# Optimization experiments

Hardware: AMD Instinct MI355X
Metric: run time of the kernel (lower is better)

## Reference

```python
import jax, jax.numpy as jnp
import numpy as np
import math

N_NODES = 50000
N_EDGES = 800000
HIDDEN = 128
NUM_GAUSS = 50
NUM_FILTERS = 128
CUTOFF = 10.0
SHIFT = math.log(2.0)


def setup_inputs() -> dict:
    key = jax.random.key(0)
    ks = jax.random.split(key, 12)
    x = jax.random.normal(ks[0], (N_NODES, HIDDEN), dtype=jnp.float32)
    edge_index = jax.random.randint(ks[1], (2, N_EDGES), 0, N_NODES, dtype=jnp.int64)
    edge_weight = jax.random.uniform(ks[2], (N_EDGES,), dtype=jnp.float32)
    edge_attr = jax.random.normal(ks[3], (N_EDGES, NUM_GAUSS), dtype=jnp.float32)
    # learned parameters (xavier-ish scale)
    def xavier(k, shape):
        fan_in, fan_out = shape[1], shape[0]
        bound = math.sqrt(6.0 / (fan_in + fan_out))
        return jax.random.uniform(k, shape, dtype=jnp.float32, minval=-bound, maxval=bound)
    mlp_w1 = xavier(ks[4], (NUM_FILTERS, NUM_GAUSS))
    mlp_b1 = jnp.zeros((NUM_FILTERS,), jnp.float32)
    mlp_w2 = xavier(ks[5], (NUM_FILTERS, NUM_FILTERS))
    mlp_b2 = jnp.zeros((NUM_FILTERS,), jnp.float32)
    lin1_w = xavier(ks[6], (NUM_FILTERS, HIDDEN))   # no bias
    lin2_w = xavier(ks[7], (HIDDEN, NUM_FILTERS))
    lin2_b = jnp.zeros((HIDDEN,), jnp.float32)
    lin_w = xavier(ks[8], (HIDDEN, HIDDEN))
    lin_b = jnp.zeros((HIDDEN,), jnp.float32)
    return {"x": x, "edge_index": edge_index, "edge_weight": edge_weight,
            "edge_attr": edge_attr, "mlp_w1": mlp_w1, "mlp_b1": mlp_b1,
            "mlp_w2": mlp_w2, "mlp_b2": mlp_b2, "lin1_w": lin1_w,
            "lin2_w": lin2_w, "lin2_b": lin2_b, "lin_w": lin_w, "lin_b": lin_b}


def shifted_softplus(v):
    return jax.nn.softplus(v) - SHIFT


def reference(x, edge_index, edge_weight, edge_attr, mlp_w1, mlp_b1,
              mlp_w2, mlp_b2, lin1_w, lin2_w, lin2_b, lin_w, lin_b):
    src, dst = edge_index[0], edge_index[1]
    # cosine cutoff per edge: [E]
    C = 0.5 * (jnp.cos(edge_weight * (jnp.pi / CUTOFF)) + 1.0)
    # edge filter MLP: [E, num_filters]
    h_e = shifted_softplus(edge_attr @ mlp_w1.T + mlp_b1)
    W = (h_e @ mlp_w2.T + mlp_b2) * C[:, None]
    # node projection, gather-multiply-scatter aggregation
    h = x @ lin1_w.T                       # [N, num_filters]
    msg = h[src] * W                       # [E, num_filters]
    agg = jax.ops.segment_sum(msg, dst, num_segments=N_NODES)  # [N, num_filters]
    h = agg @ lin2_w.T + lin2_b            # [N, hidden]
    h = shifted_softplus(h)
    out = h @ lin_w.T + lin_b              # [N, hidden]
    return out
```

## Files before the change

kernel.cpp:

```cpp
#include <hip/hip_runtime.h>
#include <hip/hip_bf16.h>
#include <math.h>

#define E_NUM 800000
#define NN 50000
#define NG 50
#define NTW (E_NUM / 16)
#define EDGE_BLOCKS 768

typedef __bf16 bf16x8 __attribute__((ext_vector_type(8)));
typedef float f32x4 __attribute__((ext_vector_type(4)));
typedef unsigned short ushortx8 __attribute__((ext_vector_type(8)));

__device__ __forceinline__ unsigned short f2b(float f) {
  union { __bf16 h; unsigned short u; } v; v.h = (__bf16)f; return v.u;
}
__device__ __forceinline__ float b2f(unsigned short u) {
  union { unsigned u; float f; } v; v.u = ((unsigned)u) << 16; return v.f;
}
__device__ __forceinline__ float sspf(float v) {
  float e = __builtin_amdgcn_exp2f(-1.4426950408889634f * fabsf(v));
  return fmaxf(v, 0.f) + 0.6931471805599453f * __builtin_amdgcn_logf(fmaf(0.5f, e, 0.5f));
}

__global__ __launch_bounds__(256) void k_hist(const int* __restrict__ ei, int* __restrict__ counts) {
  int e = blockIdx.x * 256 + threadIdx.x;
  if (e < E_NUM) atomicAdd(&counts[ei[E_NUM + e]], 1);
}

__global__ __launch_bounds__(1024) void k_scan(const int* __restrict__ counts,
                                               int* __restrict__ cursor, int* __restrict__ off) {
  __shared__ int tot[1024];
  const int t = threadIdx.x;
  const int C = (NN + 1023) >> 10;
  int lo = t * C, hi = lo + C; if (hi > NN) hi = NN; if (lo > NN) lo = NN;
  int s = 0;
  for (int i = lo; i < hi; ++i) s += counts[i];
  tot[t] = s;
  __syncthreads();
  int mine = s;
  for (int o = 1; o < 1024; o <<= 1) {
    int v = (t >= o) ? tot[t - o] : 0;
    __syncthreads();
    tot[t] += v;
    __syncthreads();
  }
  int run = tot[t] - mine;
  for (int i = lo; i < hi; ++i) { int c = counts[i]; cursor[i] = run; off[i] = run; run += c; }
  if (t == 1023) off[NN] = E_NUM;
}

__global__ __launch_bounds__(256) void k_scatter2(const int* __restrict__ ei,
                                                  int* __restrict__ cursor,
                                                  int* __restrict__ srcS, int* __restrict__ dstS,
                                                  int* __restrict__ eS) {
  int e = blockIdx.x * 256 + threadIdx.x;
  if (e < E_NUM) {
    int d = ei[E_NUM + e];
    int pos = atomicAdd(&cursor[d], 1);
    srcS[pos] = ei[e];
    dstS[pos] = d;
    eS[pos] = e;
  }
}

__global__ __launch_bounds__(256) void k_mfma_gemm(
    const float* __restrict__ X, const float* __restrict__ Wm,
    const float* __restrict__ bias, float* __restrict__ out, int act, int nrows)
{
  __shared__ __attribute__((aligned(16))) unsigned short s_x[128 * 128];
  __shared__ __attribute__((aligned(16))) unsigned short s_w[128 * 128];
  const int tid = threadIdx.x;
  const int w = tid >> 6, lane = tid & 63, q = lane >> 4, n16 = lane & 15;
  const int base = blockIdx.x * 128;

  for (int c = tid; c < 128 * 16; c += 256) {
    int f = c >> 4, ch = c & 15;
    const float4* wp = (const float4*)(Wm + f * 128 + ch * 8);
    float4 v0 = wp[0], v1 = wp[1];
    ushortx8 v = { f2b(v0.x), f2b(v0.y), f2b(v0.z), f2b(v0.w),
                   f2b(v1.x), f2b(v1.y), f2b(v1.z), f2b(v1.w) };
    *(ushortx8*)&s_w[(f << 7) + ((ch ^ (f & 15)) << 3)] = v;
  }
  for (int c = tid; c < 128 * 16; c += 256) {
    int r = c >> 4, ch = c & 15;
    int n = base + r;
    float4 v0 = {0.f, 0.f, 0.f, 0.f}, v1 = v0;
    if (n < nrows) {
      const float4* xp = (const float4*)(X + (long)n * 128 + ch * 8);
      v0 = xp[0]; v1 = xp[1];
    }
    ushortx8 v = { f2b(v0.x), f2b(v0.y), f2b(v0.z), f2b(v0.w),
                   f2b(v1.x), f2b(v1.y), f2b(v1.z), f2b(v1.w) };
    *(ushortx8*)&s_x[(r << 7) + ((ch ^ (r & 15)) << 3)] = v;
  }
  __syncthreads();

  float bv[8];
#pragma unroll
  for (int t = 0; t < 8; ++t) bv[t] = bias ? bias[t * 16 + n16] : 0.f;

  bf16x8 a[2][4];
#pragma unroll
  for (int g = 0; g < 2; ++g) {
    int r = w * 32 + g * 16 + n16;
#pragma unroll
    for (int ks = 0; ks < 4; ++ks)
      a[g][ks] = *(const bf16x8*)&s_x[(r << 7) + (((ks * 4 + q) ^ (r & 15)) << 3)];
  }
#pragma unroll
  for (int t = 0; t < 8; ++t) {
    int f = t * 16 + n16;
    bf16x8 b[4];
#pragma unroll
    for (int ks = 0; ks < 4; ++ks)
      b[ks] = *(const bf16x8*)&s_w[(f << 7) + (((ks * 4 + q) ^ (f & 15)) << 3)];
#pragma unroll
    for (int g = 0; g < 2; ++g) {
      f32x4 acc = {0.f, 0.f, 0.f, 0.f};
#pragma unroll
      for (int ks = 0; ks < 4; ++ks)
        acc = __builtin_amdgcn_mfma_f32_16x16x32_bf16(a[g][ks], b[ks], acc, 0, 0, 0);
#pragma unroll
      for (int r = 0; r < 4; ++r) {
        int n = base + w * 32 + g * 16 + q * 4 + r;
        if (n < nrows) {
          float v = acc[r] + bv[t];
          if (act) v = sspf(v);
          out[(long)n * 128 + f] = v;
        }
      }
    }
  }
}

__global__ __launch_bounds__(256, 2) void k_gemm23(
    const float* __restrict__ A, const float* __restrict__ W2,
    const float* __restrict__ B2, const float* __restrict__ W3,
    const float* __restrict__ B3, float* __restrict__ out, int nrows)
{
  __shared__ __attribute__((aligned(16))) unsigned short s_x[128 * 128];
  __shared__ __attribute__((aligned(16))) unsigned short s_w[128 * 128];
  const int tid = threadIdx.x;
  const int w = tid >> 6, lane = tid & 63, q = lane >> 4, n16 = lane & 15;
  const int base = blockIdx.x * 128;

  for (int c = tid; c < 128 * 16; c += 256) {
    int f = c >> 4, ch = c & 15;
    const float4* wp = (const float4*)(W2 + f * 128 + ch * 8);
    float4 v0 = wp[0], v1 = wp[1];
    ushortx8 v = { f2b(v0.x), f2b(v0.y), f2b(v0.z), f2b(v0.w),
                   f2b(v1.x), f2b(v1.y), f2b(v1.z), f2b(v1.w) };
    *(ushortx8*)&s_w[(f << 7) + ((ch ^ (f & 15)) << 3)] = v;
  }
  for (int c = tid; c < 128 * 16; c += 256) {
    int r = c >> 4, ch = c & 15;
    int n = base + r;
    float4 v0 = {0.f, 0.f, 0.f, 0.f}, v1 = v0;
    if (n < nrows) {
      const float4* xp = (const float4*)(A + (long)n * 128 + ch * 8);
      v0 = xp[0]; v1 = xp[1];
    }
    ushortx8 v = { f2b(v0.x), f2b(v0.y), f2b(v0.z), f2b(v0.w),
                   f2b(v1.x), f2b(v1.y), f2b(v1.z), f2b(v1.w) };
    *(ushortx8*)&s_x[(r << 7) + ((ch ^ (r & 15)) << 3)] = v;
  }
  __syncthreads();

  float b2v[8], b3v[8];
#pragma unroll
  for (int t = 0; t < 8; ++t) { b2v[t] = B2[t * 16 + n16]; b3v[t] = B3[t * 16 + n16]; }

  bf16x8 a[2][4];
#pragma unroll
  for (int g = 0; g < 2; ++g) {
    int r = w * 32 + g * 16 + n16;
#pragma unroll
    for (int ks = 0; ks < 4; ++ks)
      a[g][ks] = *(const bf16x8*)&s_x[(r << 7) + (((ks * 4 + q) ^ (r & 15)) << 3)];
  }
  float acc1[8][2][4];
#pragma unroll
  for (int t = 0; t < 8; ++t) {
    int f = t * 16 + n16;
    bf16x8 b[4];
#pragma unroll
    for (int ks = 0; ks < 4; ++ks)
      b[ks] = *(const bf16x8*)&s_w[(f << 7) + (((ks * 4 + q) ^ (f & 15)) << 3)];
#pragma unroll
    for (int g = 0; g < 2; ++g) {
      f32x4 acc = {0.f, 0.f, 0.f, 0.f};
#pragma unroll
      for (int ks = 0; ks < 4; ++ks)
        acc = __builtin_amdgcn_mfma_f32_16x16x32_bf16(a[g][ks], b[ks], acc, 0, 0, 0);
#pragma unroll
      for (int r = 0; r < 4; ++r) acc1[t][g][r] = acc[r];
    }
  }
  __syncthreads();

#pragma unroll
  for (int t = 0; t < 8; ++t) {
    int f = t * 16 + n16;
#pragma unroll
    for (int g = 0; g < 2; ++g)
#pragma unroll
      for (int r = 0; r < 4; ++r) {
        int row = w * 32 + g * 16 + q * 4 + r;
        s_x[(row << 7) + (((f >> 3) ^ (row & 15)) << 3) + (f & 7)] =
            f2b(sspf(acc1[t][g][r] + b2v[t]));
      }
  }
  for (int c = tid; c < 128 * 16; c += 256) {
    int f = c >> 4, ch = c & 15;
    const float4* wp = (const float4*)(W3 + f * 128 + ch * 8);
    float4 v0 = wp[0], v1 = wp[1];
    ushortx8 v = { f2b(v0.x), f2b(v0.y), f2b(v0.z), f2b(v0.w),
                   f2b(v1.x), f2b(v1.y), f2b(v1.z), f2b(v1.w) };
    *(ushortx8*)&s_w[(f << 7) + ((ch ^ (f & 15)) << 3)] = v;
  }
  __syncthreads();

#pragma unroll
  for (int g = 0; g < 2; ++g) {
    int r = w * 32 + g * 16 + n16;
#pragma unroll
    for (int ks = 0; ks < 4; ++ks)
      a[g][ks] = *(const bf16x8*)&s_x[(r << 7) + (((ks * 4 + q) ^ (r & 15)) << 3)];
  }
#pragma unroll
  for (int t = 0; t < 8; ++t) {
    int f = t * 16 + n16;
    bf16x8 b[4];
#pragma unroll
    for (int ks = 0; ks < 4; ++ks)
      b[ks] = *(const bf16x8*)&s_w[(f << 7) + (((ks * 4 + q) ^ (f & 15)) << 3)];
#pragma unroll
    for (int g = 0; g < 2; ++g) {
      f32x4 acc = {0.f, 0.f, 0.f, 0.f};
#pragma unroll
      for (int ks = 0; ks < 4; ++ks)
        acc = __builtin_amdgcn_mfma_f32_16x16x32_bf16(a[g][ks], b[ks], acc, 0, 0, 0);
#pragma unroll
      for (int r = 0; r < 4; ++r) {
        int n = base + w * 32 + g * 16 + q * 4 + r;
        if (n < nrows) out[(long)n * 128 + f] = acc[r] + b3v[t];
      }
    }
  }
}

__global__ __launch_bounds__(256, 3) void k_edge_agg(
    const float* __restrict__ attr, const int* __restrict__ ei,
    const float* __restrict__ ew, const float* __restrict__ w1,
    const float* __restrict__ b1, const float* __restrict__ w2,
    const float* __restrict__ b2, const float* __restrict__ h,
    const int* __restrict__ srcS, const int* __restrict__ dstS,
    const int* __restrict__ eS, float* __restrict__ agg, int mode)
{
  __shared__ __attribute__((aligned(16))) unsigned short s_w2[128 * 128];
  __shared__ __attribute__((aligned(16))) unsigned short s_scr[4 * 16 * 136];

  const int tid  = threadIdx.x;
  const int w    = tid >> 6;
  const int lane = tid & 63;
  const int q    = lane >> 4;
  const int n16  = lane & 15;

  for (int i = tid; i < 128 * 128; i += 256) {
    int f = i >> 7, k = i & 127;
    int pos = (f << 7) + ((((k >> 3) ^ (f & 15)) << 3)) + (k & 7);
    s_w2[pos] = f2b(w2[i]);
  }
  bf16x8 w1A[8], w1B[8];
#pragma unroll
  for (int t = 0; t < 8; ++t) {
    int f = t * 16 + n16;
    const float* row = w1 + f * NG;
    union { ushortx8 u; bf16x8 b; } ua, ub;
#pragma unroll
    for (int j = 0; j < 8; ++j) ua.u[j] = f2b(row[q * 8 + j]);
#pragma unroll
    for (int j = 0; j < 8; ++j) { int k = 32 + q * 8 + j; ub.u[j] = (k < NG) ? f2b(row[k]) : (unsigned short)0; }
    w1A[t] = ua.b; w1B[t] = ub.b;
  }
  float b1v[8], b2v[8];
#pragma unroll
  for (int t = 0; t < 8; ++t) {
    b1v[t] = b1[t * 16 + n16];
    b2v[t] = b2[t * 16 + n16];
  }
  __syncthreads();

  unsigned short* scr = s_scr + w * (16 * 136);
  const int nwaves = EDGE_BLOCKS * 4;
  const int gw = blockIdx.x * 4 + w;

  for (int tile = gw; tile < NTW; tile += nwaves) {
    const int e0 = tile * 16;
    const int eA = (mode == 1) ? eS[e0 + n16] : (e0 + n16);
    const float* rp = attr + (long)eA * NG;

    float2 p0 = *(const float2*)(rp + q * 8);
    float2 p1 = *(const float2*)(rp + q * 8 + 2);
    float2 p2 = *(const float2*)(rp + q * 8 + 4);
    float2 p3 = *(const float2*)(rp + q * 8 + 6);
    float2 p4 = {0.f, 0.f}, p5 = {0.f, 0.f}, p6 = {0.f, 0.f}, p7 = {0.f, 0.f};
    if (q < 2) {
      const float* rp2 = rp + 32 + q * 8;
      p4 = *(const float2*)(rp2);
      p5 = *(const float2*)(rp2 + 2);
      p6 = *(const float2*)(rp2 + 4);
      p7 = *(const float2*)(rp2 + 6);
    } else if (q == 2) {
      p4 = *(const float2*)(rp + 48);
    }
    union { ushortx8 u; bf16x8 b; } ua, ub;
    ua.u[0] = f2b(p0.x); ua.u[1] = f2b(p0.y); ua.u[2] = f2b(p1.x); ua.u[3] = f2b(p1.y);
    ua.u[4] = f2b(p2.x); ua.u[5] = f2b(p2.y); ua.u[6] = f2b(p3.x); ua.u[7] = f2b(p3.y);
    ub.u[0] = f2b(p4.x); ub.u[1] = f2b(p4.y); ub.u[2] = f2b(p5.x); ub.u[3] = f2b(p5.y);
    ub.u[4] = f2b(p6.x); ub.u[5] = f2b(p6.y); ub.u[6] = f2b(p7.x); ub.u[7] = f2b(p7.y);

#pragma unroll
    for (int t = 0; t < 8; ++t) {
      f32x4 acc = {0.f, 0.f, 0.f, 0.f};
      acc = __builtin_amdgcn_mfma_f32_16x16x32_bf16(ua.b, w1A[t], acc, 0, 0, 0);
      acc = __builtin_amdgcn_mfma_f32_16x16x32_bf16(ub.b, w1B[t], acc, 0, 0, 0);
      int f = t * 16 + n16;
#pragma unroll
      for (int r = 0; r < 4; ++r) {
        int row = q * 4 + r;
        scr[row * 136 + f] = f2b(sspf(acc[r] + b1v[t]));
      }
    }
    __builtin_amdgcn_wave_barrier();

    bf16x8 a2f[4];
#pragma unroll
    for (int ks = 0; ks < 4; ++ks)
      a2f[ks] = *(const bf16x8*)&scr[n16 * 136 + ks * 32 + q * 8];
    __builtin_amdgcn_wave_barrier();

    float cvv[4];
#pragma unroll
    for (int r = 0; r < 4; ++r) {
      int ee = (mode == 1) ? eS[e0 + q * 4 + r] : (e0 + q * 4 + r);
      cvv[r] = 0.5f * (__builtin_amdgcn_cosf(ew[ee] * 0.05f) + 1.f);
    }

    int srcv[4], dstv[4];
    if (mode == 0) {
#pragma unroll
      for (int r = 0; r < 4; ++r) {
        srcv[r] = ei[e0 + q * 4 + r];
        dstv[r] = ei[E_NUM + e0 + q * 4 + r];
      }
    }

#pragma unroll
    for (int t = 0; t < 8; ++t) {
      int f = t * 16 + n16;
      f32x4 acc = {0.f, 0.f, 0.f, 0.f};
#pragma unroll
      for (int ks = 0; ks < 4; ++ks) {
        bf16x8 bb = *(const bf16x8*)&s_w2[(f << 7) + (((ks * 4 + q) ^ (f & 15)) << 3)];
        acc = __builtin_amdgcn_mfma_f32_16x16x32_bf16(a2f[ks], bb, acc, 0, 0, 0);
      }
      if (mode == 1) {
#pragma unroll
        for (int r = 0; r < 4; ++r) {
          int row = q * 4 + r;
          scr[row * 136 + f] = f2b((acc[r] + b2v[t]) * cvv[r]);
        }
      } else {
#pragma unroll
        for (int r = 0; r < 4; ++r) {
          float msg = h[(long)srcv[r] * 128 + f] * (acc[r] + b2v[t]) * cvv[r];
          atomicAdd(&agg[(long)dstv[r] * 128 + f], msg);
        }
      }
    }

    if (mode == 1) {
      __builtin_amdgcn_wave_barrier();
      int dcur = -1, rowstart = 0;
      float ax = 0.f, ay = 0.f;
#pragma unroll
      for (int hf = 0; hf < 2; ++hf) {
        int dv[8]; float2 hv[8];
#pragma unroll
        for (int i = 0; i < 8; ++i) {
          int pos = e0 + hf * 8 + i;
          dv[i] = __builtin_amdgcn_readfirstlane(dstS[pos]);
          int sv = __builtin_amdgcn_readfirstlane(srcS[pos]);
          hv[i] = *(const float2*)(h + (long)sv * 128 + (lane << 1));
        }
#pragma unroll
        for (int i = 0; i < 8; ++i) {
          int row = hf * 8 + i;
          if (dv[i] != dcur) {
            if (dcur >= 0) {
              float* ap = agg + (long)dcur * 128 + (lane << 1);
              if (rowstart == 0) { atomicAdd(ap, ax); atomicAdd(ap + 1, ay); }
              else { float2 o; o.x = ax; o.y = ay; *(float2*)ap = o; }
            }
            dcur = dv[i]; ax = 0.f; ay = 0.f; rowstart = row;
          }
          unsigned wp = *(const unsigned*)&scr[row * 136 + (lane << 1)];
          ax = fmaf(hv[i].x, b2f((unsigned short)(wp & 0xffffu)), ax);
          ay = fmaf(hv[i].y, b2f((unsigned short)(wp >> 16)), ay);
        }
      }
      {
        float* ap = agg + (long)dcur * 128 + (lane << 1);
        atomicAdd(ap, ax); atomicAdd(ap + 1, ay);
      }
      __builtin_amdgcn_wave_barrier();
    }
  }
}

extern "C" void kernel_launch(void* const* d_in, const int* in_sizes, int n_in,
                              void* d_out, int out_size, void* d_ws, size_t ws_size,
                              hipStream_t stream) {
  const float* x     = (const float*)d_in[0];
  const int*   ei    = (const int*)  d_in[1];
  const float* ew    = (const float*)d_in[2];
  const float* attr  = (const float*)d_in[3];
  const float* w1    = (const float*)d_in[4];
  const float* b1    = (const float*)d_in[5];
  const float* w2    = (const float*)d_in[6];
  const float* b2    = (const float*)d_in[7];
  const float* lin1w = (const float*)d_in[8];
  const float* lin2w = (const float*)d_in[9];
  const float* lin2b = (const float*)d_in[10];
  const float* linw  = (const float*)d_in[11];
  const float* linb  = (const float*)d_in[12];
  float* out = (float*)d_out;

  char* base = (char*)d_ws;
  float* agg    = (float*)base;
  float* h      = agg + (size_t)NN * 128;
  int*   counts = (int*)(h + (size_t)NN * 128);
  int*   cursor = counts + NN;
  int*   off    = cursor + NN;
  int*   srcS   = off + NN + 1;
  int*   dstS   = srcS + E_NUM;
  int*   eS     = dstS + E_NUM;
  size_t need   = (size_t)((char*)(eS + E_NUM) - base);
  const int mode = (ws_size >= need) ? 1 : 0;

  const int gemm_grid = (NN + 127) / 128;
  (void)hipMemsetAsync(agg, 0, (size_t)NN * 128 * sizeof(float), stream);
  if (mode == 1) {
    (void)hipMemsetAsync(counts, 0, (size_t)NN * sizeof(int), stream);
    k_hist<<<(E_NUM + 255) / 256, 256, 0, stream>>>(ei, counts);
    k_scan<<<1, 1024, 0, stream>>>(counts, cursor, off);
    k_scatter2<<<(E_NUM + 255) / 256, 256, 0, stream>>>(ei, cursor, srcS, dstS, eS);
  }
  k_mfma_gemm<<<gemm_grid, 256, 0, stream>>>(x, lin1w, nullptr, h, 0, NN);
  k_edge_agg<<<EDGE_BLOCKS, 256, 0, stream>>>(attr, ei, ew, w1, b1, w2, b2, h,
                                              srcS, dstS, eS, agg, mode);
  k_gemm23<<<gemm_grid, 256, 0, stream>>>(agg, lin2w, lin2b, linw, linb, out, NN);
}
```

Before: 640.6 us.

## Pre-permute bf16 edge attrs and cutoff in scatter; prefetch next tile in edge kernel

The scatter pass now writes edge attributes already converted to bf16 and padded to 64 entries, along with the cosine cutoff value, in dst-sorted order. This replaces the indirect eS lookup and the strided fp32 attribute gather in the edge kernel with contiguous reads. The edge loop software-pipelines the next tile's attributes and source indices, and issues all 16 h-row gathers up front. In exchange it needs a large extra workspace and more register pressure, and if the workspace is too small the code falls back to the unsorted atomic path.

Measured after the change: 711.9 us. 1.11x slower.

```diff
diff --git a/kernel.cpp b/kernel.cpp
--- a/kernel.cpp
+++ b/kernel.cpp
@@ -29,7 +29,7 @@
 }
 
 __global__ __launch_bounds__(1024) void k_scan(const int* __restrict__ counts,
-                                               int* __restrict__ cursor, int* __restrict__ off) {
+                                               int* __restrict__ cursor) {
   __shared__ int tot[1024];
   const int t = threadIdx.x;
   const int C = (NN + 1023) >> 10;
@@ -46,21 +46,36 @@
     __syncthreads();
   }
   int run = tot[t] - mine;
-  for (int i = lo; i < hi; ++i) { int c = counts[i]; cursor[i] = run; off[i] = run; run += c; }
-  if (t == 1023) off[NN] = E_NUM;
-}
-
-__global__ __launch_bounds__(256) void k_scatter2(const int* __restrict__ ei,
-                                                  int* __restrict__ cursor,
-                                                  int* __restrict__ srcS, int* __restrict__ dstS,
-                                                  int* __restrict__ eS) {
+  for (int i = lo; i < hi; ++i) { int c = counts[i]; cursor[i] = run; run += c; }
+}
+
+__global__ __launch_bounds__(256) void k_scatter2(
+    const int* __restrict__ ei, const float* __restrict__ ew,
+    const float* __restrict__ attr, int* __restrict__ cursor,
+    int* __restrict__ srcS, int* __restrict__ dstS,
+    float* __restrict__ cS, unsigned short* __restrict__ attrS)
+{
   int e = blockIdx.x * 256 + threadIdx.x;
-  if (e < E_NUM) {
-    int d = ei[E_NUM + e];
-    int pos = atomicAdd(&cursor[d], 1);
-    srcS[pos] = ei[e];
-    dstS[pos] = d;
-    eS[pos] = e;
+  if (e >= E_NUM) return;
+  int d = ei[E_NUM + e];
+  int pos = atomicAdd(&cursor[d], 1);
+  srcS[pos] = ei[e];
+  dstS[pos] = d;
+  cS[pos] = 0.5f * (__builtin_amdgcn_cosf(ew[e] * 0.05f) + 1.f);
+  const float* rp = attr + (long)e * NG;
+  unsigned short* op = attrS + (long)pos * 64;
+  float2 v[25];
+#pragma unroll
+  for (int i = 0; i < 25; ++i) v[i] = *(const float2*)(rp + 2 * i);
+#pragma unroll
+  for (int c = 0; c < 8; ++c) {
+    ushortx8 o;
+#pragma unroll
+    for (int j = 0; j < 8; ++j) {
+      int k = c * 8 + j;
+      o[j] = (k < NG) ? f2b((k & 1) ? v[k >> 1].y : v[k >> 1].x) : (unsigned short)0;
+    }
+    *(ushortx8*)(op + c * 8) = o;
   }
 }
 
@@ -256,7 +271,8 @@
     const float* __restrict__ b1, const float* __restrict__ w2,
     const float* __restrict__ b2, const float* __restrict__ h,
     const int* __restrict__ srcS, const int* __restrict__ dstS,
-    const int* __restrict__ eS, float* __restrict__ agg, int mode)
+    const float* __restrict__ cS, const unsigned short* __restrict__ attrS,
+    float* __restrict__ agg, int mode)
 {
   __shared__ __attribute__((aligned(16))) unsigned short s_w2[128 * 128];
   __shared__ __attribute__((aligned(16))) unsigned short s_scr[4 * 16 * 136];
@@ -296,124 +312,180 @@
   const int nwaves = EDGE_BLOCKS * 4;
   const int gw = blockIdx.x * 4 + w;
 
-  for (int tile = gw; tile < NTW; tile += nwaves) {
-    const int e0 = tile * 16;
-    const int eA = (mode == 1) ? eS[e0 + n16] : (e0 + n16);
-    const float* rp = attr + (long)eA * NG;
-
-    float2 p0 = *(const float2*)(rp + q * 8);
-    float2 p1 = *(const float2*)(rp + q * 8 + 2);
-    float2 p2 = *(const float2*)(rp + q * 8 + 4);
-    float2 p3 = *(const float2*)(rp + q * 8 + 6);
-    float2 p4 = {0.f, 0.f}, p5 = {0.f, 0.f}, p6 = {0.f, 0.f}, p7 = {0.f, 0.f};
-    if (q < 2) {
-      const float* rp2 = rp + 32 + q * 8;
-      p4 = *(const float2*)(rp2);
-      p5 = *(const float2*)(rp2 + 2);
-      p6 = *(const float2*)(rp2 + 4);
-      p7 = *(const float2*)(rp2 + 6);
-    } else if (q == 2) {
-      p4 = *(const float2*)(rp + 48);
-    }
-    union { ushortx8 u; bf16x8 b; } ua, ub;
-    ua.u[0] = f2b(p0.x); ua.u[1] = f2b(p0.y); ua.u[2] = f2b(p1.x); ua.u[3] = f2b(p1.y);
-    ua.u[4] = f2b(p2.x); ua.u[5] = f2b(p2.y); ua.u[6] = f2b(p3.x); ua.u[7] = f2b(p3.y);
-    ub.u[0] = f2b(p4.x); ub.u[1] = f2b(p4.y); ub.u[2] = f2b(p5.x); ub.u[3] = f2b(p5.y);
-    ub.u[4] = f2b(p6.x); ub.u[5] = f2b(p6.y); ub.u[6] = f2b(p7.x); ub.u[7] = f2b(p7.y);
-
-#pragma unroll
-    for (int t = 0; t < 8; ++t) {
-      f32x4 acc = {0.f, 0.f, 0.f, 0.f};
-      acc = __builtin_amdgcn_mfma_f32_16x16x32_bf16(ua.b, w1A[t], acc, 0, 0, 0);
-      acc = __builtin_amdgcn_mfma_f32_16x16x32_bf16(ub.b, w1B[t], acc, 0, 0, 0);
-      int f = t * 16 + n16;
-#pragma unroll
-      for (int r = 0; r < 4; ++r) {
-        int row = q * 4 + r;
-        scr[row * 136 + f] = f2b(sspf(acc[r] + b1v[t]));
-      }
-    }
-    __builtin_amdgcn_wave_barrier();
-
-    bf16x8 a2f[4];
-#pragma unroll
-    for (int ks = 0; ks < 4; ++ks)
-      a2f[ks] = *(const bf16x8*)&scr[n16 * 136 + ks * 32 + q * 8];
-    __builtin_amdgcn_wave_barrier();
-
-    float cvv[4];
-#pragma unroll
-    for (int r = 0; r < 4; ++r) {
-      int ee = (mode == 1) ? eS[e0 + q * 4 + r] : (e0 + q * 4 + r);
-      cvv[r] = 0.5f * (__builtin_amdgcn_cosf(ew[ee] * 0.05f) + 1.f);
-    }
-
-    int srcv[4], dstv[4];
-    if (mode == 0) {
-#pragma unroll
-      for (int r = 0; r < 4; ++r) {
-        srcv[r] = ei[e0 + q * 4 + r];
-        dstv[r] = ei[E_NUM + e0 + q * 4 + r];
-      }
-    }
-
-#pragma unroll
-    for (int t = 0; t < 8; ++t) {
-      int f = t * 16 + n16;
-      f32x4 acc = {0.f, 0.f, 0.f, 0.f};
-#pragma unroll
-      for (int ks = 0; ks < 4; ++ks) {
-        bf16x8 bb = *(const bf16x8*)&s_w2[(f << 7) + (((ks * 4 + q) ^ (f & 15)) << 3)];
-        acc = __builtin_amdgcn_mfma_f32_16x16x32_bf16(a2f[ks], bb, acc, 0, 0, 0);
-      }
-      if (mode == 1) {
+  if (mode == 1) {
+    int tile = gw;
+    bf16x8 uaC, ubC;
+    int svs[16];
+    {
+      const long e0 = (long)tile * 16;
+      uaC = *(const bf16x8*)(attrS + (e0 + n16) * 64 + q * 8);
+      ubC = *(const bf16x8*)(attrS + (e0 + n16) * 64 + 32 + q * 8);
+#pragma unroll
+      for (int i = 0; i < 16; ++i) svs[i] = __builtin_amdgcn_readfirstlane(srcS[e0 + i]);
+    }
+
+    for (; tile < NTW; tile += nwaves) {
+      const int e0 = tile * 16;
+      const int tn = tile + nwaves;
+      const bool hasnext = (tn < NTW);
+
+      float2 hv[16];
+#pragma unroll
+      for (int i = 0; i < 16; ++i)
+        hv[i] = *(const float2*)(h + (long)svs[i] * 128 + (lane << 1));
+      float cvv[4];
+#pragma unroll
+      for (int r = 0; r < 4; ++r) cvv[r] = cS[e0 + q * 4 + r];
+      bf16x8 uaN = uaC, ubN = ubC;
+      int svN[16];
+#pragma unroll
+      for (int i = 0; i < 16; ++i) svN[i] = 0;
+      if (hasnext) {
+        const long en = (long)tn * 16;
+        uaN = *(const bf16x8*)(attrS + (en + n16) * 64 + q * 8);
+        ubN = *(const bf16x8*)(attrS + (en + n16) * 64 + 32 + q * 8);
+#pragma unroll
+        for (int i = 0; i < 16; ++i) svN[i] = srcS[en + i];
+      }
+
+#pragma unroll
+      for (int t = 0; t < 8; ++t) {
+        f32x4 acc = {0.f, 0.f, 0.f, 0.f};
+        acc = __builtin_amdgcn_mfma_f32_16x16x32_bf16(uaC, w1A[t], acc, 0, 0, 0);
+        acc = __builtin_amdgcn_mfma_f32_16x16x32_bf16(ubC, w1B[t], acc, 0, 0, 0);
+        int f = t * 16 + n16;
+#pragma unroll
+        for (int r = 0; r < 4; ++r) {
+          int row = q * 4 + r;
+          scr[row * 136 + f] = f2b(sspf(acc[r] + b1v[t]));
+        }
+      }
+      __builtin_amdgcn_wave_barrier();
+
+      bf16x8 a2f[4];
+#pragma unroll
+      for (int ks = 0; ks < 4; ++ks)
+        a2f[ks] = *(const bf16x8*)&scr[n16 * 136 + ks * 32 + q * 8];
+      __builtin_amdgcn_wave_barrier();
+
+#pragma unroll
+      for (int t = 0; t < 8; ++t) {
+        int f = t * 16 + n16;
+        f32x4 acc = {0.f, 0.f, 0.f, 0.f};
+#pragma unroll
+        for (int ks = 0; ks < 4; ++ks) {
+          bf16x8 bb = *(const bf16x8*)&s_w2[(f << 7) + (((ks * 4 + q) ^ (f & 15)) << 3)];
+          acc = __builtin_amdgcn_mfma_f32_16x16x32_bf16(a2f[ks], bb, acc, 0, 0, 0);
+        }
 #pragma unroll
         for (int r = 0; r < 4; ++r) {
           int row = q * 4 + r;
           scr[row * 136 + f] = f2b((acc[r] + b2v[t]) * cvv[r]);
         }
-      } else {
+      }
+      __builtin_amdgcn_wave_barrier();
+
+      int dvv[16];
+#pragma unroll
+      for (int i = 0; i < 16; ++i) dvv[i] = dstS[e0 + i];
+      int dcur = -1, rowstart = 0;
+      float ax = 0.f, ay = 0.f;
+#pragma unroll
+      for (int i = 0; i < 16; ++i) {
+        int dv = __builtin_amdgcn_readfirstlane(dvv[i]);
+        if (dv != dcur) {
+          if (dcur >= 0) {
+            float* ap = agg + (long)dcur * 128 + (lane << 1);
+            if (rowstart == 0) { atomicAdd(ap, ax); atomicAdd(ap + 1, ay); }
+            else { float2 o; o.x = ax; o.y = ay; *(float2*)ap = o; }
+          }
+          dcur = dv; ax = 0.f; ay = 0.f; rowstart = i;
+        }
+        unsigned wp = *(const unsigned*)&scr[i * 136 + (lane << 1)];
+        ax = fmaf(hv[i].x, b2f((unsigned short)(wp & 0xffffu)), ax);
+        ay = fmaf(hv[i].y, b2f((unsigned short)(wp >> 16)), ay);
+      }
+      {
+        float* ap = agg + (long)dcur * 128 + (lane << 1);
+        atomicAdd(ap, ax); atomicAdd(ap + 1, ay);
+      }
+      __builtin_amdgcn_wave_barrier();
+
+      if (hasnext) {
+#pragma unroll
+        for (int i = 0; i < 16; ++i) svs[i] = __builtin_amdgcn_readfirstlane(svN[i]);
+        uaC = uaN; ubC = ubN;
+      }
+    }
+  } else {
+    for (int tile = gw; tile < NTW; tile += nwaves) {
+      const int e0 = tile * 16;
+      const int er = e0 + n16;
+      const float* rp = attr + (long)er * NG;
+
+      float2 p0 = *(const float2*)(rp + q * 8);
+      float2 p1 = *(const float2*)(rp + q * 8 + 2);
+      float2 p2 = *(const float2*)(rp + q * 8 + 4);
+      float2 p3 = *(const float2*)(rp + q * 8 + 6);
+      float2 p4 = {0.f, 0.f}, p5 = {0.f, 0.f}, p6 = {0.f, 0.f}, p7 = {0.f, 0.f};
+      if (q < 2) {
+        const float* rp2 = rp + 32 + q * 8;
+        p4 = *(const float2*)(rp2);
+        p5 = *(const float2*)(rp2 + 2);
+        p6 = *(const float2*)(rp2 + 4);
+        p7 = *(const float2*)(rp2 + 6);
+      } else if (q == 2) {
+        p4 = *(const float2*)(rp + 48);
+      }
+      union { ushortx8 u; bf16x8 b; } ua, ub;
+      ua.u[0] = f2b(p0.x); ua.u[1] = f2b(p0.y); ua.u[2] = f2b(p1.x); ua.u[3] = f2b(p1.y);
+      ua.u[4] = f2b(p2.x); ua.u[5] = f2b(p2.y); ua.u[6] = f2b(p3.x); ua.u[7] = f2b(p3.y);
+      ub.u[0] = f2b(p4.x); ub.u[1] = f2b(p4.y); ub.u[2] = f2b(p5.x); ub.u[3] = f2b(p5.y);
+      ub.u[4] = f2b(p6.x); ub.u[5] = f2b(p6.y); ub.u[6] = f2b(p7.x); ub.u[7] = f2b(p7.y);
+
+#pragma unroll
+      for (int t = 0; t < 8; ++t) {
+        f32x4 acc = {0.f, 0.f, 0.f, 0.f};
+        acc = __builtin_amdgcn_mfma_f32_16x16x32_bf16(ua.b, w1A[t], acc, 0, 0, 0);
+        acc = __builtin_amdgcn_mfma_f32_16x16x32_bf16(ub.b, w1B[t], acc, 0, 0, 0);
+        int f = t * 16 + n16;
+#pragma unroll
+        for (int r = 0; r < 4; ++r) {
+          int row = q * 4 + r;
+          scr[row * 136 + f] = f2b(sspf(acc[r] + b1v[t]));
+        }
+      }
+      __builtin_amdgcn_wave_barrier();
+
+      bf16x8 a2f[4];
+#pragma unroll
+      for (int ks = 0; ks < 4; ++ks)
+        a2f[ks] = *(const bf16x8*)&scr[n16 * 136 + ks * 32 + q * 8];
+      __builtin_amdgcn_wave_barrier();
+
+      float cvv[4];
+      int srcv[4], dstv[4];
+#pragma unroll
+      for (int r = 0; r < 4; ++r) {
+        cvv[r] = 0.5f * (__builtin_amdgcn_cosf(ew[e0 + q * 4 + r] * 0.05f) + 1.f);
+        srcv[r] = ei[e0 + q * 4 + r];
+        dstv[r] = ei[E_NUM + e0 + q * 4 + r];
+      }
+
+#pragma unroll
+      for (int t = 0; t < 8; ++t) {
+        int f = t * 16 + n16;
+        f32x4 acc = {0.f, 0.f, 0.f, 0.f};
+#pragma unroll
+        for (int ks = 0; ks < 4; ++ks) {
+          bf16x8 bb = *(const bf16x8*)&s_w2[(f << 7) + (((ks * 4 + q) ^ (f & 15)) << 3)];
+          acc = __builtin_amdgcn_mfma_f32_16x16x32_bf16(a2f[ks], bb, acc, 0, 0, 0);
+        }
 #pragma unroll
         for (int r = 0; r < 4; ++r) {
           float msg = h[(long)srcv[r] * 128 + f] * (acc[r] + b2v[t]) * cvv[r];
           atomicAdd(&agg[(long)dstv[r] * 128 + f], msg);
         }
-      }
-    }
-
-    if (mode == 1) {
-      __builtin_amdgcn_wave_barrier();
-      int dcur = -1, rowstart = 0;
-      float ax = 0.f, ay = 0.f;
-#pragma unroll
-      for (int hf = 0; hf < 2; ++hf) {
-        int dv[8]; float2 hv[8];
-#pragma unroll
-        for (int i = 0; i < 8; ++i) {
-          int pos = e0 + hf * 8 + i;
-          dv[i] = __builtin_amdgcn_readfirstlane(dstS[pos]);
-          int sv = __builtin_amdgcn_readfirstlane(srcS[pos]);
-          hv[i] = *(const float2*)(h + (long)sv * 128 + (lane << 1));
-        }
-#pragma unroll
-        for (int i = 0; i < 8; ++i) {
-          int row = hf * 8 + i;
-          if (dv[i] != dcur) {
-            if (dcur >= 0) {
-              float* ap = agg + (long)dcur * 128 + (lane << 1);
-              if (rowstart == 0) { atomicAdd(ap, ax); atomicAdd(ap + 1, ay); }
-              else { float2 o; o.x = ax; o.y = ay; *(float2*)ap = o; }
-            }
-            dcur = dv[i]; ax = 0.f; ay = 0.f; rowstart = row;
-          }
-          unsigned wp = *(const unsigned*)&scr[row * 136 + (lane << 1)];
-          ax = fmaf(hv[i].x, b2f((unsigned short)(wp & 0xffffu)), ax);
-          ay = fmaf(hv[i].y, b2f((unsigned short)(wp >> 16)), ay);
-        }
-      }
-      {
-        float* ap = agg + (long)dcur * 128 + (lane << 1);
-        atomicAdd(ap, ax); atomicAdd(ap + 1, ay);
       }
       __builtin_amdgcn_wave_barrier();
     }
@@ -443,11 +515,13 @@
   float* h      = agg + (size_t)NN * 128;
   int*   counts = (int*)(h + (size_t)NN * 128);
   int*   cursor = counts + NN;
-  int*   off    = cursor + NN;
-  int*   srcS   = off + NN + 1;
+  int*   srcS   = cursor + NN;
   int*   dstS   = srcS + E_NUM;
-  int*   eS     = dstS + E_NUM;
-  size_t need   = (size_t)((char*)(eS + E_NUM) - base);
+  float* cS     = (float*)(dstS + E_NUM);
+  size_t head   = (size_t)((char*)(cS + E_NUM) - base);
+  size_t aoff   = (head + 255) & ~(size_t)255;
+  unsigned short* attrS = (unsigned short*)(base + aoff);
+  size_t need   = aoff + (size_t)E_NUM * 64 * sizeof(unsigned short);
   const int mode = (ws_size >= need) ? 1 : 0;
 
   const int gemm_grid = (NN + 127) / 128;
@@ -455,11 +529,12 @@
   if (mode == 1) {
     (void)hipMemsetAsync(counts, 0, (size_t)NN * sizeof(int), stream);
     k_hist<<<(E_NUM + 255) / 256, 256, 0, stream>>>(ei, counts);
-    k_scan<<<1, 1024, 0, stream>>>(counts, cursor, off);
-    k_scatter2<<<(E_NUM + 255) / 256, 256, 0, stream>>>(ei, cursor, srcS, dstS, eS);
+    k_scan<<<1, 1024, 0, stream>>>(counts, cursor);
+    k_scatter2<<<(E_NUM + 255) / 256, 256, 0, stream>>>(ei, ew, attr, cursor,
+                                                        srcS, dstS, cS, attrS);
   }
   k_mfma_gemm<<<gemm_grid, 256, 0, stream>>>(x, lin1w, nullptr, h, 0, NN);
   k_edge_agg<<<EDGE_BLOCKS, 256, 0, stream>>>(attr, ei, ew, w1, b1, w2, b2, h,
-                                              srcS, dstS, eS, agg, mode);
+                                              srcS, dstS, cS, attrS, agg, mode);
   k_gemm23<<<gemm_grid, 256, 0, stream>>>(agg, lin2w, lin2b, linw, linb, out, NN);
 }
```
